# Optimization experiments

Hardware: AMD Instinct MI355X
Metric: run time of the kernel (lower is better)

## Reference

```python
import jax, jax.numpy as jnp
import numpy as np

B, C, H, W, D = 4, 64, 64, 64, 4
CQ = C // 8  # query/key channels


def setup_inputs() -> dict:
    key = jax.random.key(0)
    ks = jax.random.split(key, 10)
    x2d = jax.random.normal(ks[0], (B, C, H, W, D), dtype=jnp.float32)
    x3d = jax.random.normal(ks[1], (B, C, H, W, D), dtype=jnp.float32)
    # 1x1 Conv3d weights collapsed to (out_ch, in_ch) matrices + biases
    Wq = jax.random.normal(ks[2], (CQ, C), dtype=jnp.float32) * 0.05
    bq = jax.random.normal(ks[3], (CQ,), dtype=jnp.float32) * 0.05
    Wk = jax.random.normal(ks[4], (CQ, C), dtype=jnp.float32) * 0.05
    bk = jax.random.normal(ks[5], (CQ,), dtype=jnp.float32) * 0.05
    Wv = jax.random.normal(ks[6], (C, C), dtype=jnp.float32) * 0.05
    bv = jax.random.normal(ks[7], (C,), dtype=jnp.float32) * 0.05
    gamma = jax.random.normal(ks[8], (1,), dtype=jnp.float32)
    return {"x2d": x2d, "x3d": x3d, "Wq": Wq, "bq": bq, "Wk": Wk,
            "bk": bk, "Wv": Wv, "bv": bv, "gamma": gamma}


def _conv1x1(Wmat, bias, x):
    # x: (B, C, D, H, W); 1x1x1 Conv3d == channel matmul
    y = jnp.einsum('oc,bcdhw->bodhw', Wmat, x)
    return y + bias[None, :, None, None, None]


def reference(x2d, x3d, Wq, bq, Wk, bk, Wv, bv, gamma):
    x = jnp.transpose(x2d, (0, 1, 4, 2, 3))  # (B, C, D, H, W)
    b, c, d, h, w = x.shape
    n = h * w
    q = _conv1x1(Wq, bq, x).reshape(b, -1, n)   # (B, CQ*D, N)
    k = _conv1x1(Wk, bk, x).reshape(b, -1, n)   # (B, CQ*D, N)
    v = _conv1x1(Wv, bv, x).reshape(b, -1, n)   # (B, C*D, N)
    energy = jnp.einsum('bkn,bkm->bnm', q, k)   # (B, N, N), no scaling (faithful)
    attn = jax.nn.softmax(energy, axis=-1)
    # out[b,c,i] = sum_j attn[b,i,j] * v[b,c,j]
    out = jnp.einsum('bcm,bnm->bcn', v, attn)
    out = out.reshape(b, c, d, h, w)
    out = jnp.transpose(out, (0, 1, 3, 4, 2))   # back to (B, C, H, W, D)
    return gamma * out + x3d
```

## Files before the change

kernel.cpp:

```cpp
#include <hip/hip_runtime.h>
#include <hip/hip_bf16.h>

#define CH 64
#define NN 4096
#define SS 16384

typedef __attribute__((ext_vector_type(8))) short bf16x8;
typedef __attribute__((ext_vector_type(4))) float f32x4;

#define QB_OFF 0
#define KB_OFF 524288
#define VT_OFF 1048576

static __device__ __forceinline__ ushort bfbits(float x) {
    __hip_bfloat16 h = __float2bfloat16(x);
    return *(ushort*)&h;
}

static __device__ __forceinline__ void gld_lds16(const ushort* g, ushort* l) {
    __builtin_amdgcn_global_load_lds(
        (const __attribute__((address_space(1))) void*)g,
        (__attribute__((address_space(3))) void*)l, 16, 0, 0);
}

__global__ __launch_bounds__(256) void qkv_kernel(
    const float* __restrict__ x,
    const float* __restrict__ Wq, const float* __restrict__ bq,
    const float* __restrict__ Wk, const float* __restrict__ bk,
    const float* __restrict__ Wv, const float* __restrict__ bv,
    ushort* __restrict__ qb, ushort* __restrict__ kb, ushort* __restrict__ vt)
{
    __shared__ __align__(16) ushort Tqk[128 * 40];
    __shared__ __align__(16) ushort Tv[80 * 144];

    const int blk = blockIdx.x;
    const int b = blk >> 7, sup = (blk >> 2) & 31, og = blk & 3;
    const int tid = threadIdx.x;
    const int nl = tid >> 2, d = tid & 3;

    const int vcnt = (og < 2) ? 12 : 20;
    const int vo0 = (og == 0) ? 0 : (og == 1) ? 12 : (og == 2) ? 24 : 44;

    const float* xb = x + (size_t)b * CH * SS + sup * 512;

    for (int t = 0; t < 2; ++t) {
        const float* xp = xb + t * 256 + tid;
        float xr[CH];
#pragma unroll
        for (int c = 0; c < CH; ++c) xr[c] = xp[(size_t)c * SS];

        const int slot = 32 * (nl >> 4) + 8 * ((nl >> 2) & 3) + 4 * t + (nl & 3);

        if (og < 2) {
            const float* Wqk = (og == 0) ? Wq : Wk;
            const float* bqk = (og == 0) ? bq : bk;
            ushort* trow = &Tqk[(t * 64 + nl) * 40 + d];
#pragma unroll
            for (int o = 0; o < 8; o += 2) {
                float a0 = bqk[o], a1 = bqk[o + 1];
#pragma unroll
                for (int c = 0; c < CH; ++c) {
                    a0 = fmaf(Wqk[o * CH + c],       xr[c], a0);
                    a1 = fmaf(Wqk[(o + 1) * CH + c], xr[c], a1);
                }
                trow[o * 4]       = bfbits(a0);
                trow[(o + 1) * 4] = bfbits(a1);
            }
        }
        ushort* vcol = &Tv[d * 144 + slot];
        const float* Wvb = Wv + vo0 * CH;
        const float* bvb = bv + vo0;
        if (og < 2) {
#pragma unroll
            for (int j = 0; j < 12; j += 2) {
                float a0 = bvb[j], a1 = bvb[j + 1];
#pragma unroll
                for (int c = 0; c < CH; ++c) {
                    a0 = fmaf(Wvb[j * CH + c],       xr[c], a0);
                    a1 = fmaf(Wvb[(j + 1) * CH + c], xr[c], a1);
                }
                vcol[(j * 4) * 144]       = bfbits(a0);
                vcol[((j + 1) * 4) * 144] = bfbits(a1);
            }
        } else {
#pragma unroll
            for (int j = 0; j < 20; j += 2) {
                float a0 = bvb[j], a1 = bvb[j + 1];
#pragma unroll
                for (int c = 0; c < CH; ++c) {
                    a0 = fmaf(Wvb[j * CH + c],       xr[c], a0);
                    a1 = fmaf(Wvb[(j + 1) * CH + c], xr[c], a1);
                }
                vcol[(j * 4) * 144]       = bfbits(a0);
                vcol[((j + 1) * 4) * 144] = bfbits(a1);
            }
        }
    }
    __syncthreads();

    if (og < 2) {
        ushort* dst = (og == 0 ? qb : kb);
#pragma unroll
        for (int jj = 0; jj < 2; ++jj) {
            int idx = jj * 256 + tid;
            int row = idx >> 2, seg = idx & 3;
            *(uint4*)(dst + ((size_t)(b * NN + sup * 128 + row)) * 32 + seg * 8)
                = *(const uint4*)&Tqk[row * 40 + seg * 8];
        }
    }
    const int nchunks = vcnt * 64;
    ushort* vout = vt + ((size_t)((b * 32 + sup) * 256 + vo0 * 4)) * 144;
#pragma unroll
    for (int j = 0; j < 5; ++j) {
        int idx = j * 256 + tid;
        if (idx < nchunks) {
            int row = idx >> 4, seg = idx & 15;
            *(uint4*)(vout + (size_t)row * 144 + seg * 8)
                = *(const uint4*)&Tv[row * 144 + seg * 8];
        }
    }
}

__global__ __launch_bounds__(256, 2) void flash_kernel(
    const ushort* __restrict__ qb, const ushort* __restrict__ kb,
    const ushort* __restrict__ vt, const float* __restrict__ x3d,
    const float* __restrict__ gptr, float* __restrict__ out)
{
    __shared__ __align__(16) ushort Vls[2][128 * 144];
    __shared__ float lbuf[4 * 4 * 16];

    const int tid = threadIdx.x;
    const int g   = blockIdx.x & 7;
    const int b   = g >> 1;
    const int cvh = g & 1;
    const int r0  = (blockIdx.x >> 3) << 6;
    const int w = tid >> 6, lane = tid & 63, q = lane >> 4, l15 = lane & 15;

    bf16x8 Qf[4];
#pragma unroll
    for (int rt = 0; rt < 4; ++rt)
        Qf[rt] = *(const bf16x8*)(qb + (size_t)(b * NN + r0 + 16 * rt + l15) * 32 + 8 * q);

    f32x4 acc[8][4];
#pragma unroll
    for (int i = 0; i < 8; ++i)
#pragma unroll
        for (int j = 0; j < 4; ++j) acc[i][j] = (f32x4){0.f, 0.f, 0.f, 0.f};
    float l_acc[4] = {0.f, 0.f, 0.f, 0.f};

    const ushort* kgl = kb + (size_t)b * NN * 32 + (16 * w + l15) * 32 + 8 * q;

    const ushort* vgl = vt + ((size_t)(b * 32) * 256 + 128 * cvh) * 144;

#pragma unroll
    for (int i = 0; i < 9; ++i)
        gld_lds16(vgl + (size_t)(i * 256 + tid) * 8,
                  (ushort*)Vls[0] + (i * 256 + tid) * 8);

    bf16x8 Kn0 = *(const bf16x8*)(kgl);
    bf16x8 Kn1 = *(const bf16x8*)(kgl + 2048);

    for (int pt = 0; pt < 32; ++pt) {
        __syncthreads();
        if (pt < 31) {
            const ushort* src = vgl + (size_t)(pt + 1) * 36864;
            ushort* dst = (ushort*)Vls[(pt + 1) & 1];
#pragma unroll
            for (int i = 0; i < 9; ++i)
                gld_lds16(src + (size_t)(i * 256 + tid) * 8, dst + (i * 256 + tid) * 8);
        }
        bf16x8 Ka0 = Kn0, Ka1 = Kn1;
        if (pt < 31) {
            Kn0 = *(const bf16x8*)(kgl + (size_t)(2 * pt + 2) * 2048);
            Kn1 = *(const bf16x8*)(kgl + (size_t)(2 * pt + 3) * 2048);
        }

        f32x4 S0[4], S1[4];
#pragma unroll
        for (int rt = 0; rt < 4; ++rt)
            S0[rt] = __builtin_amdgcn_mfma_f32_16x16x32_bf16(
                Ka0, Qf[rt], (f32x4){0.f, 0.f, 0.f, 0.f}, 0, 0, 0);
#pragma unroll
        for (int rt = 0; rt < 4; ++rt)
            S1[rt] = __builtin_amdgcn_mfma_f32_16x16x32_bf16(
                Ka1, Qf[rt], (f32x4){0.f, 0.f, 0.f, 0.f}, 0, 0, 0);

        bf16x8 Pb[4];
#pragma unroll
        for (int rt = 0; rt < 4; ++rt) {
            float e0 = __expf(S0[rt][0]), e1 = __expf(S0[rt][1]);
            float e2 = __expf(S0[rt][2]), e3 = __expf(S0[rt][3]);
            float f0 = __expf(S1[rt][0]), f1 = __expf(S1[rt][1]);
            float f2 = __expf(S1[rt][2]), f3 = __expf(S1[rt][3]);
            l_acc[rt] += ((e0 + e1) + (e2 + e3)) + ((f0 + f1) + (f2 + f3));
            union { bf16x8 v; __hip_bfloat162 h[4]; } u;
            u.h[0] = __float22bfloat162_rn(make_float2(e0, e1));
            u.h[1] = __float22bfloat162_rn(make_float2(e2, e3));
            u.h[2] = __float22bfloat162_rn(make_float2(f0, f1));
            u.h[3] = __float22bfloat162_rn(make_float2(f2, f3));
            Pb[rt] = u.v;
        }

        const ushort* vb = Vls[pt & 1] + 32 * w + 8 * q;
#pragma unroll
        for (int cvt = 0; cvt < 8; ++cvt) {
            bf16x8 Va = *(const bf16x8*)(vb + (16 * cvt + l15) * 144);
#pragma unroll
            for (int rt = 0; rt < 4; ++rt)
                acc[cvt][rt] = __builtin_amdgcn_mfma_f32_16x16x32_bf16(
                    Va, Pb[rt], acc[cvt][rt], 0, 0, 0);
        }
    }

#pragma unroll
    for (int rt = 0; rt < 4; ++rt) {
        float v = l_acc[rt];
        v += __shfl_xor(v, 16);
        v += __shfl_xor(v, 32);
        if (lane < 16) lbuf[(w * 4 + rt) * 16 + lane] = v;
    }
    __syncthreads();
    const float linv = 1.f / (lbuf[(0 + w) * 16 + l15] + lbuf[(4 + w) * 16 + l15] +
                              lbuf[(8 + w) * 16 + l15] + lbuf[(12 + w) * 16 + l15]);
    const float gl = gptr[0] * linv;

    f32x4* Obuf = (f32x4*)&Vls[0][0];
#pragma unroll
    for (int cvt = 0; cvt < 8; ++cvt) {
        __syncthreads();
#pragma unroll
        for (int rt = 0; rt < 4; ++rt)
            Obuf[(w * 64 + lane) * 5 + rt] = acc[cvt][rt];
        __syncthreads();
        f32x4 o = Obuf[lane * 5 + w];
        o += Obuf[(64 + lane) * 5 + w];
        o += Obuf[(128 + lane) * 5 + w];
        o += Obuf[(192 + lane) * 5 + w];
        size_t addr = ((size_t)(b * CH + 32 * cvh + 4 * cvt + q) * NN
                       + (r0 + 16 * w + l15)) * 4;
        float4 xr = *(const float4*)(x3d + addr);
        float4 res;
        res.x = fmaf(gl, o[0], xr.x);
        res.y = fmaf(gl, o[1], xr.y);
        res.z = fmaf(gl, o[2], xr.z);
        res.w = fmaf(gl, o[3], xr.w);
        *(float4*)(out + addr) = res;
    }
}

extern "C" void kernel_launch(void* const* d_in, const int* in_sizes, int n_in,
                              void* d_out, int out_size, void* d_ws, size_t ws_size,
                              hipStream_t stream)
{
    const float* x2d = (const float*)d_in[0];
    const float* x3d = (const float*)d_in[1];
    const float* Wq  = (const float*)d_in[2];
    const float* bq  = (const float*)d_in[3];
    const float* Wk  = (const float*)d_in[4];
    const float* bk  = (const float*)d_in[5];
    const float* Wv  = (const float*)d_in[6];
    const float* bv  = (const float*)d_in[7];
    const float* gma = (const float*)d_in[8];

    ushort* wsb = (ushort*)d_ws;

    qkv_kernel<<<512, 256, 0, stream>>>(x2d, Wq, bq, Wk, bk, Wv, bv,
                                        wsb + QB_OFF, wsb + KB_OFF, wsb + VT_OFF);
    flash_kernel<<<512, 256, 0, stream>>>(wsb + QB_OFF, wsb + KB_OFF, wsb + VT_OFF,
                                          x3d, gma, (float*)d_out);
}
```

Before: 169.5 us.

## Compute all Q, K, V channels per thread in QKV projection, dropping LDS staging

```diff
diff --git a/kernel.cpp b/kernel.cpp
--- a/kernel.cpp
+++ b/kernel.cpp
@@ -30,94 +30,42 @@
     const float* __restrict__ Wv, const float* __restrict__ bv,
     ushort* __restrict__ qb, ushort* __restrict__ kb, ushort* __restrict__ vt)
 {
-    __shared__ __align__(16) ushort Tqk[128 * 40];
-    __shared__ __align__(16) ushort Tv[80 * 144];
-
-    const int blk = blockIdx.x;
-    const int b = blk >> 7, sup = (blk >> 2) & 31, og = blk & 3;
-    const int tid = threadIdx.x;
-    const int nl = tid >> 2, d = tid & 3;
-
-    const int vcnt = (og < 2) ? 12 : 20;
-    const int vo0 = (og == 0) ? 0 : (og == 1) ? 12 : (og == 2) ? 24 : 44;
-
-    const float* xb = x + (size_t)b * CH * SS + sup * 512;
-
-    for (int t = 0; t < 2; ++t) {
-        const float* xp = xb + t * 256 + tid;
-        float xr[CH];
-#pragma unroll
-        for (int c = 0; c < CH; ++c) xr[c] = xp[(size_t)c * SS];
-
-        const int slot = 32 * (nl >> 4) + 8 * ((nl >> 2) & 3) + 4 * t + (nl & 3);
-
-        if (og < 2) {
-            const float* Wqk = (og == 0) ? Wq : Wk;
-            const float* bqk = (og == 0) ? bq : bk;
-            ushort* trow = &Tqk[(t * 64 + nl) * 40 + d];
-#pragma unroll
-            for (int o = 0; o < 8; o += 2) {
-                float a0 = bqk[o], a1 = bqk[o + 1];
-#pragma unroll
-                for (int c = 0; c < CH; ++c) {
-                    a0 = fmaf(Wqk[o * CH + c],       xr[c], a0);
-                    a1 = fmaf(Wqk[(o + 1) * CH + c], xr[c], a1);
-                }
-                trow[o * 4]       = bfbits(a0);
-                trow[(o + 1) * 4] = bfbits(a1);
-            }
-        }
-        ushort* vcol = &Tv[d * 144 + slot];
-        const float* Wvb = Wv + vo0 * CH;
-        const float* bvb = bv + vo0;
-        if (og < 2) {
-#pragma unroll
-            for (int j = 0; j < 12; j += 2) {
-                float a0 = bvb[j], a1 = bvb[j + 1];
-#pragma unroll
-                for (int c = 0; c < CH; ++c) {
-                    a0 = fmaf(Wvb[j * CH + c],       xr[c], a0);
-                    a1 = fmaf(Wvb[(j + 1) * CH + c], xr[c], a1);
-                }
-                vcol[(j * 4) * 144]       = bfbits(a0);
-                vcol[((j + 1) * 4) * 144] = bfbits(a1);
-            }
-        } else {
-#pragma unroll
-            for (int j = 0; j < 20; j += 2) {
-                float a0 = bvb[j], a1 = bvb[j + 1];
-#pragma unroll
-                for (int c = 0; c < CH; ++c) {
-                    a0 = fmaf(Wvb[j * CH + c],       xr[c], a0);
-                    a1 = fmaf(Wvb[(j + 1) * CH + c], xr[c], a1);
-                }
-                vcol[(j * 4) * 144]       = bfbits(a0);
-                vcol[((j + 1) * 4) * 144] = bfbits(a1);
-            }
-        }
-    }
-    __syncthreads();
-
-    if (og < 2) {
-        ushort* dst = (og == 0 ? qb : kb);
-#pragma unroll
-        for (int jj = 0; jj < 2; ++jj) {
-            int idx = jj * 256 + tid;
-            int row = idx >> 2, seg = idx & 3;
-            *(uint4*)(dst + ((size_t)(b * NN + sup * 128 + row)) * 32 + seg * 8)
-                = *(const uint4*)&Tqk[row * 40 + seg * 8];
-        }
-    }
-    const int nchunks = vcnt * 64;
-    ushort* vout = vt + ((size_t)((b * 32 + sup) * 256 + vo0 * 4)) * 144;
-#pragma unroll
-    for (int j = 0; j < 5; ++j) {
-        int idx = j * 256 + tid;
-        if (idx < nchunks) {
-            int row = idx >> 4, seg = idx & 15;
-            *(uint4*)(vout + (size_t)row * 144 + seg * 8)
-                = *(const uint4*)&Tv[row * 144 + seg * 8];
-        }
+    const int gid = blockIdx.x * 256 + threadIdx.x;
+    const int b = gid >> 14;
+    const int s = gid & (SS - 1);
+    const int n = s >> 2;
+    const int d = s & 3;
+    const float* xp = x + (size_t)b * CH * SS + s;
+    float xr[CH];
+#pragma unroll
+    for (int c = 0; c < CH; ++c) xr[c] = xp[(size_t)c * SS];
+
+    ushort* qo = qb + (size_t)(b * NN + n) * 32 + d;
+#pragma unroll
+    for (int o = 0; o < 8; ++o) {
+        float a = bq[o];
+#pragma unroll
+        for (int c = 0; c < CH; ++c) a = fmaf(Wq[o * CH + c], xr[c], a);
+        qo[o * 4] = bfbits(a);
+    }
+    ushort* ko = kb + (size_t)(b * NN + n) * 32 + d;
+#pragma unroll
+    for (int o = 0; o < 8; ++o) {
+        float a = bk[o];
+#pragma unroll
+        for (int c = 0; c < CH; ++c) a = fmaf(Wk[o * CH + c], xr[c], a);
+        ko[o * 4] = bfbits(a);
+    }
+    const int sup = n >> 7, nl = n & 127;
+    const int t = nl >> 6, nl6 = nl & 63;
+    const int slot = 32 * (nl6 >> 4) + 8 * ((nl6 >> 2) & 3) + 4 * t + (nl6 & 3);
+    ushort* vo = vt + ((size_t)((b * 32 + sup) * 256 + d)) * 144 + slot;
+#pragma unroll 8
+    for (int o = 0; o < CH; ++o) {
+        float a = bv[o];
+#pragma unroll
+        for (int c = 0; c < CH; ++c) a = fmaf(Wv[o * CH + c], xr[c], a);
+        vo[(size_t)(o * 4) * 144] = bfbits(a);
     }
 }
 
@@ -264,7 +212,7 @@
 
     ushort* wsb = (ushort*)d_ws;
 
-    qkv_kernel<<<512, 256, 0, stream>>>(x2d, Wq, bq, Wk, bk, Wv, bv,
+    qkv_kernel<<<256, 256, 0, stream>>>(x2d, Wq, bq, Wk, bk, Wv, bv,
                                         wsb + QB_OFF, wsb + KB_OFF, wsb + VT_OFF);
     flash_kernel<<<512, 256, 0, stream>>>(wsb + QB_OFF, wsb + KB_OFF, wsb + VT_OFF,
                                           x3d, gma, (float*)d_out);
```

Measured after the change: 193.1 us. 13.9% more time.
